# Kernel optimization log

Hardware: AMD Instinct MI355X
Metric: run time of the kernel (lower is better)

Reference implementation:

```python
import jax, jax.numpy as jnp
import numpy as np

GMIN = 0.01
GMAX = 10.0


def _ptanh(x, eta):
    # printed tanh-style learnable activation: eta0 + eta1 * tanh((x - eta2) * eta3)
    return eta[0] + eta[1] * jnp.tanh((x - eta[2]) * eta[3])


def setup_inputs() -> dict:
    key = jax.random.key(0)
    k1, k2 = jax.random.split(key)
    B, n_in, n_out = 32768, 256, 256
    a_previous = jax.random.uniform(k1, (B, n_in), dtype=jnp.float32)
    eta_act = jnp.array([0.0, 1.0, 0.5, 2.0], dtype=jnp.float32)
    eta_inv = jnp.array([1.0, -1.0, 0.5, 2.0], dtype=jnp.float32)
    # theta init exactly as in pLayer.__init__
    theta = jax.random.uniform(k2, (n_in + 2, n_out), dtype=jnp.float32) / 100.0 + GMIN
    theta = theta.at[-1, :].add(GMAX)
    ratio = eta_act[2] / (1.0 - eta_act[2])  # eta2/(1-eta2)
    theta = theta.at[-2, :].set(ratio * (jnp.sum(theta[:-2, :], axis=0) + theta[-1, :]))
    return {"a_previous": a_previous, "theta_": theta, "eta_act": eta_act, "eta_inv": eta_inv}


def reference(a_previous, theta_, eta_act, eta_inv):
    # clamp + threshold-to-zero (forward value of the straight-through theta)
    theta = jnp.clip(theta_, -GMAX, GMAX)
    theta = jnp.where(jnp.abs(theta) < GMIN, 0.0, theta)
    # normalized conductance weights
    abs_t = jnp.abs(theta)
    W = abs_t / jnp.sum(abs_t, axis=0, keepdims=True)  # [n_in+2, n_out]
    pos = (theta >= 0.0).astype(theta.dtype)
    neg = 1.0 - pos
    B = a_previous.shape[0]
    ones = jnp.ones((B, 1), dtype=a_previous.dtype)
    zeros = jnp.zeros((B, 1), dtype=a_previous.dtype)
    a_ext = jnp.concatenate([a_previous, ones, zeros], axis=1)  # [B, n_in+2]
    a_neg = _ptanh(a_ext, eta_inv).at[:, -1].set(0.0)  # inverter, last (dummy) col zeroed
    z = a_ext @ (W * pos) + a_neg @ (W * neg)  # [B, n_out]
    return _ptanh(z, eta_act)
```

## Files before the change

kernel.cpp:

```cpp
#include <hip/hip_runtime.h>
#include <hip/hip_bf16.h>

typedef unsigned int u32;
typedef __attribute__((ext_vector_type(8))) _Float16 f16x8;
typedef __attribute__((ext_vector_type(4))) float f32x4;

#define GMIN_ 0.01f
#define GMAX_ 10.0f

__device__ __forceinline__ float tanh_fast2(float y2) {
    float e = __expf(y2);
    float r = __builtin_amdgcn_rcpf(e + 1.0f);
    return fmaf(-2.0f, r, 1.0f);
}

__global__ __launch_bounds__(256) void prep_weights(
    const float* __restrict__ theta, const float* __restrict__ eta_inv,
    _Float16* __restrict__ W2t, float* __restrict__ bias)
{
    const int n = blockIdx.x;
    const int t = threadIdx.x;
    const int lane = t & 63, wave = t >> 6;
    __shared__ float red[4];

    float tt = theta[t * 256 + n];
    tt = fminf(fmaxf(tt, -GMAX_), GMAX_);
    if (fabsf(tt) < GMIN_) tt = 0.f;

    float extra = 0.f;
    if (t < 2) {
        extra = theta[(256 + t) * 256 + n];
        extra = fminf(fmaxf(extra, -GMAX_), GMAX_);
        if (fabsf(extra) < GMIN_) extra = 0.f;
    }

    float s = fabsf(tt) + fabsf(extra);
#pragma unroll
    for (int i = 32; i > 0; i >>= 1) s += __shfl_xor(s, i);
    if (lane == 0) red[wave] = s;
    __syncthreads();
    const float inv = 1.0f / (red[0] + red[1] + red[2] + red[3]);

    const float w  = fabsf(tt) * inv;
    const float wp = (tt >= 0.f) ? w : 0.f;
    const float wn = w - wp;
    union { _Float16 h[2]; u32 u; } p;
    p.h[0] = (_Float16)wp;
    p.h[1] = (_Float16)wn;
    *(u32*)((char*)W2t + (size_t)n * 1024 + (size_t)t * 4) = p.u;

    if (t == 0) {
        const float w6  = fabsf(extra) * inv;
        const float wp6 = (extra >= 0.f) ? w6 : 0.f;
        const float wn6 = w6 - wp6;
        const float ei0 = eta_inv[0], ei1 = eta_inv[1], ei2 = eta_inv[2], ei3 = eta_inv[3];
        const float a1  = ei0 + ei1 * tanhf((1.0f - ei2) * ei3);
        bias[n] = wp6 + a1 * wn6;
    }
}

__global__ __launch_bounds__(256, 4) void plax_gemm(
    const float* __restrict__ A, const _Float16* __restrict__ W2t,
    const float* __restrict__ bias, const float* __restrict__ eta_act,
    const float* __restrict__ eta_inv, float* __restrict__ out)
{
    const int t    = threadIdx.x;
    const int bid  = blockIdx.x;
    const int swz  = ((bid & 7) << 7) | (bid >> 3);
    const int mblk = swz >> 2;
    const int nblk = swz & 3;
    const int lane = t & 63, wave = t >> 6;
    const int lr   = lane & 15, lg = lane >> 4;

    const float ei0 = eta_inv[0], ei1 = eta_inv[1];
    const float k2i = 2.0f * eta_inv[3];
    const float c2i = 2.0f * eta_inv[2] * eta_inv[3];

    const int row0 = mblk * 128 + wave * 32;
    const int col0 = nblk * 64;

    const float*    ap = A   + (size_t)(row0 + lr) * 256 + lg * 4;
    const _Float16* bp = W2t + (size_t)(col0 + lr) * 512 + lg * 8;

    f32x4 acc[2][4] = {};

#define LD(ks, aa, bb) do {                                   \
        aa[0] = *(const float4*)(ap + (ks) * 16);             \
        aa[1] = *(const float4*)(ap + 4096 + (ks) * 16);      \
        bb[0] = *(const f16x8*)(bp + (ks) * 32);              \
        bb[1] = *(const f16x8*)(bp + 8192  + (ks) * 32);      \
        bb[2] = *(const f16x8*)(bp + 16384 + (ks) * 32);      \
        bb[3] = *(const f16x8*)(bp + 24576 + (ks) * 32);      \
    } while (0)

    float4 a4c[2]; f16x8 bfc[4];
    LD(0, a4c, bfc);

#pragma unroll
    for (int ks = 0; ks < 16; ++ks) {
        float4 a4n[2]; f16x8 bfn[4];
        if (ks < 15) LD(ks + 1, a4n, bfn);

        f16x8 af[2];
#pragma unroll
        for (int m = 0; m < 2; ++m) {
            const float4 v = a4c[m];
            f16x8 h;
            h[0] = (_Float16)v.x;
            h[1] = (_Float16)fmaf(ei1, tanh_fast2(fmaf(v.x, k2i, -c2i)), ei0);
            h[2] = (_Float16)v.y;
            h[3] = (_Float16)fmaf(ei1, tanh_fast2(fmaf(v.y, k2i, -c2i)), ei0);
            h[4] = (_Float16)v.z;
            h[5] = (_Float16)fmaf(ei1, tanh_fast2(fmaf(v.z, k2i, -c2i)), ei0);
            h[6] = (_Float16)v.w;
            h[7] = (_Float16)fmaf(ei1, tanh_fast2(fmaf(v.w, k2i, -c2i)), ei0);
            af[m] = h;
        }

#pragma unroll
        for (int m = 0; m < 2; ++m)
#pragma unroll
            for (int n = 0; n < 4; ++n)
                acc[m][n] = __builtin_amdgcn_mfma_f32_16x16x32_f16(
                    af[m], bfc[n], acc[m][n], 0, 0, 0);

        if (ks < 15) {
#pragma unroll
            for (int m = 0; m < 2; ++m) a4c[m] = a4n[m];
#pragma unroll
            for (int n = 0; n < 4; ++n) bfc[n] = bfn[n];
        }
    }
#undef LD

    const float ea0 = eta_act[0], ea1 = eta_act[1];
    const float k2a = 2.0f * eta_act[3];
    const float c2a = 2.0f * eta_act[2] * eta_act[3];

    float bc[4];
#pragma unroll
    for (int n = 0; n < 4; ++n) bc[n] = bias[col0 + n * 16 + lr];

#pragma unroll
    for (int m = 0; m < 2; ++m) {
        const int rgb = row0 + m * 16 + lg * 4;
#pragma unroll
        for (int n = 0; n < 4; ++n) {
            const int cg = col0 + n * 16 + lr;
#pragma unroll
            for (int j = 0; j < 4; ++j) {
                const float z = acc[m][n][j] + bc[n];
                out[(size_t)(rgb + j) * 256 + cg] =
                    fmaf(ea1, tanh_fast2(fmaf(z, k2a, -c2a)), ea0);
            }
        }
    }
}

extern "C" void kernel_launch(void* const* d_in, const int* in_sizes, int n_in,
                              void* d_out, int out_size, void* d_ws, size_t ws_size,
                              hipStream_t stream) {
    (void)in_sizes; (void)n_in; (void)out_size; (void)ws_size;
    const float* a       = (const float*)d_in[0];
    const float* theta   = (const float*)d_in[1];
    const float* eta_act = (const float*)d_in[2];
    const float* eta_inv = (const float*)d_in[3];
    float* out = (float*)d_out;

    _Float16* W2t  = (_Float16*)d_ws;
    float*    bias = (float*)((char*)d_ws + 256 * 512 * 2);

    prep_weights<<<256, 256, 0, stream>>>(theta, eta_inv, W2t, bias);
    plax_gemm<<<1024, 256, 0, stream>>>(a, W2t, bias, eta_act, eta_inv, out);
}
```

Before: 129.2 us.

## Stage weights in swizzled LDS and widen N tile to 128 columns

```diff
diff --git a/kernel.cpp b/kernel.cpp
--- a/kernel.cpp
+++ b/kernel.cpp
@@ -59,16 +59,18 @@
     }
 }
 
-__global__ __launch_bounds__(256, 4) void plax_gemm(
+__global__ __launch_bounds__(256, 2) void plax_gemm(
     const float* __restrict__ A, const _Float16* __restrict__ W2t,
     const float* __restrict__ bias, const float* __restrict__ eta_act,
     const float* __restrict__ eta_inv, float* __restrict__ out)
 {
+    __shared__ __align__(16) char Bs[65536];
+
     const int t    = threadIdx.x;
     const int bid  = blockIdx.x;
-    const int swz  = ((bid & 7) << 7) | (bid >> 3);
-    const int mblk = swz >> 2;
-    const int nblk = swz & 3;
+    const int swz  = ((bid & 7) << 6) | (bid >> 3);
+    const int mblk = swz >> 1;
+    const int nblk = swz & 1;
     const int lane = t & 63, wave = t >> 6;
     const int lr   = lane & 15, lg = lane >> 4;
 
@@ -77,34 +79,57 @@
     const float c2i = 2.0f * eta_inv[2] * eta_inv[3];
 
     const int row0 = mblk * 128 + wave * 32;
-    const int col0 = nblk * 64;
-
-    const float*    ap = A   + (size_t)(row0 + lr) * 256 + lg * 4;
-    const _Float16* bp = W2t + (size_t)(col0 + lr) * 512 + lg * 8;
-
-    f32x4 acc[2][4] = {};
-
-#define LD(ks, aa, bb) do {                                   \
-        aa[0] = *(const float4*)(ap + (ks) * 16);             \
-        aa[1] = *(const float4*)(ap + 4096 + (ks) * 16);      \
-        bb[0] = *(const f16x8*)(bp + (ks) * 32);              \
-        bb[1] = *(const f16x8*)(bp + 8192  + (ks) * 32);      \
-        bb[2] = *(const f16x8*)(bp + 16384 + (ks) * 32);      \
-        bb[3] = *(const f16x8*)(bp + 24576 + (ks) * 32);      \
+    const int col0 = nblk * 128;
+
+    const float* ap = A + (size_t)(row0 + lr) * 256 + lg * 4;
+
+    f32x4 acc[2][8] = {};
+
+#define LDA(it, dst) do {                                         \
+        dst[0] = *(const float4*)(ap + (it) * 16);                \
+        dst[1] = *(const float4*)(ap + 4096 + (it) * 16);         \
     } while (0)
 
-    float4 a4c[2]; f16x8 bfc[4];
-    LD(0, a4c, bfc);
-
-#pragma unroll
-    for (int ks = 0; ks < 16; ++ks) {
-        float4 a4n[2]; f16x8 bfn[4];
-        if (ks < 15) LD(ks + 1, a4n, bfn);
+    float4 aq0[2], aq1[2], aq2[2];
+    LDA(0, aq0);
+    LDA(1, aq1);
+
+    const int r_st   = t >> 5;
+    const int s_phys = t & 31;
+
+#pragma unroll
+    for (int it = 0; it < 16; ++it) {
+        const int half = it >> 3;
+        const int ks   = it & 7;
+
+        if (ks == 0) {
+            __syncthreads();
+#pragma unroll
+            for (int i = 0; i < 16; ++i) {
+                const int r  = i * 8 + r_st;
+                const int sl = (s_phys & ~7) | ((s_phys ^ r) & 7);
+                const char* gp = (const char*)W2t
+                    + (size_t)(col0 + r) * 1024 + half * 512 + sl * 16;
+                __builtin_amdgcn_global_load_lds(
+                    (const __attribute__((address_space(1))) u32*)gp,
+                    (__attribute__((address_space(3))) u32*)(Bs + i * 4096 + t * 16),
+                    16, 0, 0);
+            }
+            __syncthreads();
+        }
+
+        if (it + 2 < 16) {
+            if ((it % 3) == 0)      LDA(it + 2, aq2);
+            else if ((it % 3) == 1) LDA(it + 2, aq0);
+            else                    LDA(it + 2, aq1);
+        }
+
+        float4* acur = ((it % 3) == 0) ? aq0 : ((it % 3) == 1) ? aq1 : aq2;
 
         f16x8 af[2];
 #pragma unroll
         for (int m = 0; m < 2; ++m) {
-            const float4 v = a4c[m];
+            const float4 v = acur[m];
             f16x8 h;
             h[0] = (_Float16)v.x;
             h[1] = (_Float16)fmaf(ei1, tanh_fast2(fmaf(v.x, k2i, -c2i)), ei0);
@@ -117,35 +142,37 @@
             af[m] = h;
         }
 
+        f16x8 bf[8];
+#pragma unroll
+        for (int n = 0; n < 8; ++n) {
+            const int r  = n * 16 + lr;
+            const int s  = ks * 4 + lg;
+            const int sw = (s & ~7) | ((s ^ r) & 7);
+            bf[n] = *(const f16x8*)(Bs + (size_t)r * 512 + sw * 16);
+        }
+
 #pragma unroll
         for (int m = 0; m < 2; ++m)
 #pragma unroll
-            for (int n = 0; n < 4; ++n)
+            for (int n = 0; n < 8; ++n)
                 acc[m][n] = __builtin_amdgcn_mfma_f32_16x16x32_f16(
-                    af[m], bfc[n], acc[m][n], 0, 0, 0);
-
-        if (ks < 15) {
-#pragma unroll
-            for (int m = 0; m < 2; ++m) a4c[m] = a4n[m];
-#pragma unroll
-            for (int n = 0; n < 4; ++n) bfc[n] = bfn[n];
-        }
-    }
-#undef LD
+                    af[m], bf[n], acc[m][n], 0, 0, 0);
+    }
+#undef LDA
 
     const float ea0 = eta_act[0], ea1 = eta_act[1];
     const float k2a = 2.0f * eta_act[3];
     const float c2a = 2.0f * eta_act[2] * eta_act[3];
 
-    float bc[4];
-#pragma unroll
-    for (int n = 0; n < 4; ++n) bc[n] = bias[col0 + n * 16 + lr];
+    float bc[8];
+#pragma unroll
+    for (int n = 0; n < 8; ++n) bc[n] = bias[col0 + n * 16 + lr];
 
 #pragma unroll
     for (int m = 0; m < 2; ++m) {
         const int rgb = row0 + m * 16 + lg * 4;
 #pragma unroll
-        for (int n = 0; n < 4; ++n) {
+        for (int n = 0; n < 8; ++n) {
             const int cg = col0 + n * 16 + lr;
 #pragma unroll
             for (int j = 0; j < 4; ++j) {
@@ -171,5 +198,5 @@
     float*    bias = (float*)((char*)d_ws + 256 * 512 * 2);
 
     prep_weights<<<256, 256, 0, stream>>>(theta, eta_inv, W2t, bias);
-    plax_gemm<<<1024, 256, 0, stream>>>(a, W2t, bias, eta_act, eta_inv, out);
-}
+    plax_gemm<<<512, 256, 0, stream>>>(a, W2t, bias, eta_act, eta_inv, out);
+}
```

Measured after the change: 106.3 us. 1.22x faster.

## Stage weight tiles in swizzled LDS with double buffering; coalesce weight prep

Applied to the files above, without the earlier changes.

```diff
diff --git a/kernel.cpp b/kernel.cpp
--- a/kernel.cpp
+++ b/kernel.cpp
@@ -18,44 +18,63 @@
     const float* __restrict__ theta, const float* __restrict__ eta_inv,
     _Float16* __restrict__ W2t, float* __restrict__ bias)
 {
-    const int n = blockIdx.x;
-    const int t = threadIdx.x;
-    const int lane = t & 63, wave = t >> 6;
-    __shared__ float red[4];
-
-    float tt = theta[t * 256 + n];
-    tt = fminf(fmaxf(tt, -GMAX_), GMAX_);
-    if (fabsf(tt) < GMIN_) tt = 0.f;
-
-    float extra = 0.f;
-    if (t < 2) {
-        extra = theta[(256 + t) * 256 + n];
-        extra = fminf(fmaxf(extra, -GMAX_), GMAX_);
-        if (fabsf(extra) < GMIN_) extra = 0.f;
-    }
-
-    float s = fabsf(tt) + fabsf(extra);
-#pragma unroll
-    for (int i = 32; i > 0; i >>= 1) s += __shfl_xor(s, i);
-    if (lane == 0) red[wave] = s;
+    __shared__ float tile[258][17];
+    __shared__ float psum[16][17];
+    __shared__ float cinv[16];
+
+    const int t  = threadIdx.x;
+    const int kq = t >> 4;
+    const int nl = t & 15;
+    const int n  = blockIdx.x * 16 + nl;
+
+    float part = 0.f;
+#pragma unroll
+    for (int i = 0; i < 17; ++i) {
+        const int k = i * 16 + kq;
+        if (k < 258) {
+            float tt = theta[k * 256 + n];
+            tt = fminf(fmaxf(tt, -GMAX_), GMAX_);
+            if (fabsf(tt) < GMIN_) tt = 0.f;
+            tile[k][nl] = tt;
+            part += fabsf(tt);
+        }
+    }
+    psum[kq][nl] = part;
     __syncthreads();
-    const float inv = 1.0f / (red[0] + red[1] + red[2] + red[3]);
-
-    const float w  = fabsf(tt) * inv;
-    const float wp = (tt >= 0.f) ? w : 0.f;
-    const float wn = w - wp;
-    union { _Float16 h[2]; u32 u; } p;
-    p.h[0] = (_Float16)wp;
-    p.h[1] = (_Float16)wn;
-    *(u32*)((char*)W2t + (size_t)n * 1024 + (size_t)t * 4) = p.u;
-
-    if (t == 0) {
-        const float w6  = fabsf(extra) * inv;
-        const float wp6 = (extra >= 0.f) ? w6 : 0.f;
-        const float wn6 = w6 - wp6;
+    if (kq == 0) {
+        float s = 0.f;
+#pragma unroll
+        for (int j = 0; j < 16; ++j) s += psum[j][nl];
+        cinv[nl] = 1.0f / s;
+    }
+    __syncthreads();
+
+    const int nw = t >> 4;
+    const int kc = t & 15;
+    const float inv = cinv[nw];
+    const int nn = blockIdx.x * 16 + nw;
+#pragma unroll
+    for (int c = 0; c < 4; ++c) {
+        f16x8 h;
+#pragma unroll
+        for (int e = 0; e < 4; ++e) {
+            const float tt = tile[kc * 16 + c * 4 + e][nw];
+            const float w  = fabsf(tt) * inv;
+            const float wp = (tt >= 0.f) ? w : 0.f;
+            h[2 * e]     = (_Float16)wp;
+            h[2 * e + 1] = (_Float16)(w - wp);
+        }
+        *(f16x8*)(W2t + (size_t)nn * 512 + kc * 32 + c * 8) = h;
+    }
+
+    if (t < 16) {
+        const float tt = tile[256][t];
+        const float w  = fabsf(tt) * cinv[t];
+        const float wp = (tt >= 0.f) ? w : 0.f;
+        const float wn = w - wp;
         const float ei0 = eta_inv[0], ei1 = eta_inv[1], ei2 = eta_inv[2], ei3 = eta_inv[3];
         const float a1  = ei0 + ei1 * tanhf((1.0f - ei2) * ei3);
-        bias[n] = wp6 + a1 * wn6;
+        bias[blockIdx.x * 16 + t] = wp + a1 * wn;
     }
 }
 
@@ -64,6 +83,8 @@
     const float* __restrict__ bias, const float* __restrict__ eta_act,
     const float* __restrict__ eta_inv, float* __restrict__ out)
 {
+    __shared__ __align__(16) char Bs[2][16384];
+
     const int t    = threadIdx.x;
     const int bid  = blockIdx.x;
     const int swz  = ((bid & 7) << 7) | (bid >> 3);
@@ -79,59 +100,99 @@
     const int row0 = mblk * 128 + wave * 32;
     const int col0 = nblk * 64;
 
-    const float*    ap = A   + (size_t)(row0 + lr) * 256 + lg * 4;
-    const _Float16* bp = W2t + (size_t)(col0 + lr) * 512 + lg * 8;
+    const float* ap = A + (size_t)(row0 + lr) * 256 + lg * 4;
+
+    const _Float16* bsrc[4];
+    char*           bdst[4];
+#pragma unroll
+    for (int q = 0; q < 4; ++q) {
+        const int idx  = q * 256 + t;
+        const int col  = idx >> 4;
+        const int slot = idx & 15;
+        bsrc[q] = W2t + (size_t)(col0 + col) * 512 + slot * 8;
+        bdst[q] = (char*)&Bs[0][0] + col * 256 + ((slot ^ (col & 15)) * 16);
+    }
 
     f32x4 acc[2][4] = {};
 
-#define LD(ks, aa, bb) do {                                   \
-        aa[0] = *(const float4*)(ap + (ks) * 16);             \
-        aa[1] = *(const float4*)(ap + 4096 + (ks) * 16);      \
-        bb[0] = *(const f16x8*)(bp + (ks) * 32);              \
-        bb[1] = *(const f16x8*)(bp + 8192  + (ks) * 32);      \
-        bb[2] = *(const f16x8*)(bp + 16384 + (ks) * 32);      \
-        bb[3] = *(const f16x8*)(bp + 24576 + (ks) * 32);      \
+#define LDA(it, dst) do {                                         \
+        dst[0] = *(const float4*)(ap + (it) * 16);                \
+        dst[1] = *(const float4*)(ap + 4096 + (it) * 16);         \
     } while (0)
 
-    float4 a4c[2]; f16x8 bfc[4];
-    LD(0, a4c, bfc);
-
-#pragma unroll
-    for (int ks = 0; ks < 16; ++ks) {
-        float4 a4n[2]; f16x8 bfn[4];
-        if (ks < 15) LD(ks + 1, a4n, bfn);
-
-        f16x8 af[2];
-#pragma unroll
-        for (int m = 0; m < 2; ++m) {
-            const float4 v = a4c[m];
-            f16x8 h;
-            h[0] = (_Float16)v.x;
-            h[1] = (_Float16)fmaf(ei1, tanh_fast2(fmaf(v.x, k2i, -c2i)), ei0);
-            h[2] = (_Float16)v.y;
-            h[3] = (_Float16)fmaf(ei1, tanh_fast2(fmaf(v.y, k2i, -c2i)), ei0);
-            h[4] = (_Float16)v.z;
-            h[5] = (_Float16)fmaf(ei1, tanh_fast2(fmaf(v.z, k2i, -c2i)), ei0);
-            h[6] = (_Float16)v.w;
-            h[7] = (_Float16)fmaf(ei1, tanh_fast2(fmaf(v.w, k2i, -c2i)), ei0);
-            af[m] = h;
-        }
-
-#pragma unroll
-        for (int m = 0; m < 2; ++m)
-#pragma unroll
-            for (int n = 0; n < 4; ++n)
-                acc[m][n] = __builtin_amdgcn_mfma_f32_16x16x32_f16(
-                    af[m], bfc[n], acc[m][n], 0, 0, 0);
-
-        if (ks < 15) {
-#pragma unroll
-            for (int m = 0; m < 2; ++m) a4c[m] = a4n[m];
-#pragma unroll
-            for (int n = 0; n < 4; ++n) bfc[n] = bfn[n];
-        }
-    }
-#undef LD
+    float4 aqA[2], aqB[2];
+    LDA(0, aqA);
+
+    f16x8 breg[4];
+#pragma unroll
+    for (int q = 0; q < 4; ++q) breg[q] = *(const f16x8*)(bsrc[q]);
+#pragma unroll
+    for (int q = 0; q < 4; ++q) *(f16x8*)(bdst[q]) = breg[q];
+    asm volatile("s_waitcnt lgkmcnt(0)" ::: "memory");
+    __builtin_amdgcn_sched_barrier(0);
+    __builtin_amdgcn_s_barrier();
+
+#pragma unroll
+    for (int r = 0; r < 4; ++r) {
+        if (r < 3) {
+#pragma unroll
+            for (int q = 0; q < 4; ++q)
+                breg[q] = *(const f16x8*)(bsrc[q] + (r + 1) * 128);
+        }
+
+        const char* buf = (const char*)&Bs[r & 1][0];
+#pragma unroll
+        for (int j = 0; j < 4; ++j) {
+            const int it = r * 4 + j;
+            if (it + 1 < 16) {
+                if (it & 1) LDA(it + 1, aqA); else LDA(it + 1, aqB);
+            }
+            const float4* acur = (it & 1) ? aqB : aqA;
+
+            f16x8 af[2];
+#pragma unroll
+            for (int m = 0; m < 2; ++m) {
+                const float4 v = acur[m];
+                f16x8 h;
+                h[0] = (_Float16)v.x;
+                h[1] = (_Float16)fmaf(ei1, tanh_fast2(fmaf(v.x, k2i, -c2i)), ei0);
+                h[2] = (_Float16)v.y;
+                h[3] = (_Float16)fmaf(ei1, tanh_fast2(fmaf(v.y, k2i, -c2i)), ei0);
+                h[4] = (_Float16)v.z;
+                h[5] = (_Float16)fmaf(ei1, tanh_fast2(fmaf(v.z, k2i, -c2i)), ei0);
+                h[6] = (_Float16)v.w;
+                h[7] = (_Float16)fmaf(ei1, tanh_fast2(fmaf(v.w, k2i, -c2i)), ei0);
+                af[m] = h;
+            }
+
+            f16x8 bf[4];
+#pragma unroll
+            for (int n = 0; n < 4; ++n) {
+                const int rr   = n * 16 + lr;
+                const int phys = (j * 4 + lg) ^ (rr & 15);
+                bf[n] = *(const f16x8*)(buf + rr * 256 + phys * 16);
+            }
+
+#pragma unroll
+            for (int m = 0; m < 2; ++m)
+#pragma unroll
+                for (int n = 0; n < 4; ++n)
+                    acc[m][n] = __builtin_amdgcn_mfma_f32_16x16x32_f16(
+                        af[m], bf[n], acc[m][n], 0, 0, 0);
+        }
+
+        if (r < 3) {
+            __builtin_amdgcn_s_barrier();
+            const int off = ((r + 1) & 1) * 16384;
+#pragma unroll
+            for (int q = 0; q < 4; ++q)
+                *(f16x8*)(bdst[q] + off) = breg[q];
+            asm volatile("s_waitcnt lgkmcnt(0)" ::: "memory");
+            __builtin_amdgcn_sched_barrier(0);
+            __builtin_amdgcn_s_barrier();
+        }
+    }
+#undef LDA
 
     const float ea0 = eta_act[0], ea1 = eta_act[1];
     const float k2a = 2.0f * eta_act[3];
@@ -170,6 +231,6 @@
     _Float16* W2t  = (_Float16*)d_ws;
     float*    bias = (float*)((char*)d_ws + 256 * 512 * 2);
 
-    prep_weights<<<256, 256, 0, stream>>>(theta, eta_inv, W2t, bias);
+    prep_weights<<<16, 256, 0, stream>>>(theta, eta_inv, W2t, bias);
     plax_gemm<<<1024, 256, 0, stream>>>(a, W2t, bias, eta_act, eta_inv, out);
 }
```

After: 110.5 us. 1.17x faster.
